# Optimization experiments

Hardware: AMD Instinct MI355X
Metric: run time of the kernel (lower is better)

Reference implementation:

```python
import jax, jax.numpy as jnp
import numpy as np

OUT_FEATURES = 4096
IN_FEATURES = 4096
SCALE_EPS = 1e-5


def setup_inputs() -> dict:
    key = jax.random.key(0)
    k1, k2, k3 = jax.random.split(key, 3)
    x = jax.random.normal(k1, (8192, IN_FEATURES), dtype=jnp.float32)
    # packed int4 weights: two signed nibbles per byte-equivalent int
    weight_packed = jax.random.randint(k2, (OUT_FEATURES, IN_FEATURES // 2), 0, 256, dtype=jnp.int32)
    weight_scale = jax.random.uniform(k3, (OUT_FEATURES,), dtype=jnp.float32) * 0.01 + 1e-4
    return {"x": x, "weight_packed": weight_packed, "weight_scale": weight_scale}


def _unpack_int4(weight_packed):
    # low nibble first, then high nibble, sign-extended from 4 bits
    low = weight_packed & 15
    high = (weight_packed >> 4) & 15
    low = jnp.where(low > 7, low - 16, low)
    high = jnp.where(high > 7, high - 16, high)
    # interleave -> [out_features, in_features]
    w_q = jnp.stack([low, high], axis=-1).reshape(weight_packed.shape[0], -1)
    return w_q


def reference(x, weight_packed, weight_scale):
    # per-row activation quantization to int4 range [-8, 7]
    x_max = jnp.max(jnp.abs(x), axis=-1, keepdims=True)
    x_scale = jnp.maximum(x_max / 7.0, SCALE_EPS)          # [tokens, 1]
    x_q = jnp.clip(jnp.round(x / x_scale), -8.0, 7.0)      # float carrier of int4 values

    w_q = _unpack_int4(weight_packed).astype(jnp.float32)  # [out, in]

    out = jnp.einsum('ti,oi->to', x_q, w_q)                # [tokens, out]
    out = out * (x_scale * weight_scale[None, :])
    return out.astype(x.dtype)
```

## Files before the change

kernel.cpp:

```cpp
#include <hip/hip_runtime.h>

#define SCALE_EPS 1e-5f

typedef int v4i __attribute__((ext_vector_type(4)));

static __device__ __forceinline__ void gll16(const void* g, void* l) {
  __builtin_amdgcn_global_load_lds(
      (const __attribute__((address_space(1))) unsigned int*)g,
      (__attribute__((address_space(3))) unsigned int*)l,
      16, 0, 0);
}

__global__ __launch_bounds__(256) void unpack_w(const int* __restrict__ wp,
                                                char* __restrict__ wq) {
  const int kc = blockIdx.x;
  const int nt = blockIdx.y;
  const int tid = threadIdx.x;
  char* tile = wq + ((size_t)nt * 64 + kc) * 8192;
  const int n0 = nt * 128;
#pragma unroll
  for (int j = 0; j < 4; ++j) {
    int u = j * 256 + tid;
    int r = u >> 3;
    int p = u & 7;
    const v4i* src = (const v4i*)((const char*)wp + (size_t)(n0 + r) * 8192 + kc * 128 + p * 16);
    v4i v = *src;
    unsigned int b[8];
#pragma unroll
    for (int q = 0; q < 4; ++q) {
      int lo = ((v[q] & 15) ^ 8) - 8;
      int hi = (((v[q] >> 4) & 15) ^ 8) - 8;
      b[q * 2]     = (unsigned int)(lo & 255);
      b[q * 2 + 1] = (unsigned int)(hi & 255);
    }
    unsigned int w0 = b[0] | (b[1] << 8) | (b[2] << 16) | (b[3] << 24);
    unsigned int w1 = b[4] | (b[5] << 8) | (b[6] << 16) | (b[7] << 24);
    *(uint2*)(tile + (r >> 4) * 1024 + (p >> 1) * 256 + (r & 15) * 16 + (p & 1) * 8) =
        make_uint2(w0, w1);
  }
}

__global__ __launch_bounds__(256) void quant_x(const float* __restrict__ x,
                                               char* __restrict__ xq,
                                               float* __restrict__ xs) {
  __shared__ float lmax[4][4];
  const int tid = threadIdx.x;
  const int w = tid >> 6;
  const int l = tid & 63;
  const int t0 = blockIdx.x * 4;
  const int row = l >> 4;
  const int t = t0 + row;
  const int sub = l & 15;

  const float* base = x + (size_t)t * 4096 + w * 1024 + sub * 4;
  float4 vals[16];
  float m = 0.0f;
#pragma unroll
  for (int s = 0; s < 16; ++s) {
    vals[s] = *(const float4*)(base + s * 64);
    m = fmaxf(m, fmaxf(fmaxf(fabsf(vals[s].x), fabsf(vals[s].y)),
                       fmaxf(fabsf(vals[s].z), fabsf(vals[s].w))));
  }
#pragma unroll
  for (int d = 1; d < 16; d <<= 1) m = fmaxf(m, __shfl_xor(m, d, 64));
  if (sub == 0) lmax[w][row] = m;
  __syncthreads();
  float rm = fmaxf(fmaxf(lmax[0][row], lmax[1][row]),
                   fmaxf(lmax[2][row], lmax[3][row]));
  float scale = fmaxf(rm / 7.0f, SCALE_EPS);
  if (w == 0 && sub == 0) xs[t] = scale;

  const int mt = t0 >> 7;
  const int f = (t0 & 127) >> 4;
  const int r16 = t & 15;
  const int cc = sub >> 2;
  const int b4 = (sub & 3) * 4;

#pragma unroll
  for (int s = 0; s < 16; ++s) {
    float4 v = vals[s];
    int q0 = (int)fminf(fmaxf(rintf(v.x / scale), -8.0f), 7.0f);
    int q1 = (int)fminf(fmaxf(rintf(v.y / scale), -8.0f), 7.0f);
    int q2 = (int)fminf(fmaxf(rintf(v.z / scale), -8.0f), 7.0f);
    int q3 = (int)fminf(fmaxf(rintf(v.w / scale), -8.0f), 7.0f);
    unsigned int wd = (unsigned int)(q0 & 255) | ((unsigned int)(q1 & 255) << 8) |
                      ((unsigned int)(q2 & 255) << 16) | ((unsigned int)(q3 & 255) << 24);
    *(unsigned int*)(xq + ((size_t)mt * 64 + w * 16 + s) * 8192 +
                     f * 1024 + cc * 256 + r16 * 16 + b4) = wd;
  }
}

__global__ __launch_bounds__(512, 2) void gemm_i8(const char* __restrict__ xq,
                                                  const char* __restrict__ wq,
                                                  const float* __restrict__ xs,
                                                  const float* __restrict__ wsc,
                                                  float* __restrict__ out) {
  __shared__ char lds[4][32768];
  const int tid = threadIdx.x;
  const int wid = tid >> 6;
  const int lane = tid & 63;
  const int wm = wid >> 2;
  const int wn = wid & 3;

  const int bid = blockIdx.x;
  const int wg = (bid & 7) * 64 + (bid >> 3);
  const int by = wg >> 4;
  const int bx = wg & 15;

  const char* Asrc0 = xq + (size_t)(2 * by) * 64 * 8192;
  const char* Asrc1 = Asrc0 + 64 * 8192;
  const char* Bsrc0 = wq + (size_t)(2 * bx) * 64 * 8192;
  const char* Bsrc1 = Bsrc0 + 64 * 8192;
  const int toff = tid * 16;

  v4i acc[8][4] = {};
  v4i fB[2][4];
  v4i aA0, aA1, aA2, aA3;

#define STAGE4(kt)                                                      \
  do {                                                                  \
    char* dst_ = lds[(kt) & 3] + toff;                                  \
    gll16(Asrc0 + (size_t)(kt) * 8192 + toff, dst_);                    \
    gll16(Asrc1 + (size_t)(kt) * 8192 + toff, dst_ + 8192);             \
    gll16(Bsrc0 + (size_t)(kt) * 8192 + toff, dst_ + 16384);            \
    gll16(Bsrc1 + (size_t)(kt) * 8192 + toff, dst_ + 24576);            \
  } while (0)

#define MF2(m0, m1, x, y, c)                                                          \
  do {                                                                                \
    __builtin_amdgcn_s_setprio(1);                                                    \
    _Pragma("unroll") for (int ni = 0; ni < 4; ++ni) {                                \
      acc[m0][ni] =                                                                   \
          __builtin_amdgcn_mfma_i32_16x16x64_i8(x, fB[c][ni], acc[m0][ni], 0, 0, 0);  \
      acc[m1][ni] =                                                                   \
          __builtin_amdgcn_mfma_i32_16x16x64_i8(y, fB[c][ni], acc[m1][ni], 0, 0, 0);  \
    }                                                                                 \
    __builtin_amdgcn_s_setprio(0);                                                    \
  } while (0)

#define TILE(c, kt, do_stage, do_next, vm)                                   \
  do {                                                                       \
    const char* As_ = lds[(kt) & 3] + wm * 8192 + lane * 16;                 \
    const char* Bn_ = lds[((kt) + 1) & 3] + 16384 + wn * 4096 + lane * 16;   \
    const char* An_ = lds[((kt) + 1) & 3] + wm * 8192 + lane * 16;           \
                                 \
    aA2 = *(const v4i*)(As_ + 2048);                                         \
    aA3 = *(const v4i*)(As_ + 3072);                                         \
    MF2(0, 1, aA0, aA1, c);                                                  \
                                 \
    aA0 = *(const v4i*)(As_ + 4096);                                         \
    aA1 = *(const v4i*)(As_ + 5120);                                         \
    MF2(2, 3, aA2, aA3, c);                                                  \
                      \
    if ((vm) == 4) asm volatile("s_waitcnt vmcnt(4)" ::: "memory");          \
    else if ((vm) == 0) asm volatile("s_waitcnt vmcnt(0)" ::: "memory");     \
    __builtin_amdgcn_s_barrier();                                            \
    __builtin_amdgcn_sched_barrier(0);                                       \
       \
    if (do_stage) STAGE4((kt) + 3);                                          \
    aA2 = *(const v4i*)(As_ + 6144);                                         \
    aA3 = *(const v4i*)(As_ + 7168);                                         \
    if (do_next) {                                                           \
      fB[1 - (c)][0] = *(const v4i*)(Bn_);                                   \
      fB[1 - (c)][1] = *(const v4i*)(Bn_ + 1024);                            \
    }                                                                        \
    MF2(4, 5, aA0, aA1, c);                                                  \
             \
    if (do_next) {                                                           \
      fB[1 - (c)][2] = *(const v4i*)(Bn_ + 2048);                            \
      fB[1 - (c)][3] = *(const v4i*)(Bn_ + 3072);                            \
      aA0 = *(const v4i*)(An_);                                              \
      aA1 = *(const v4i*)(An_ + 1024);                                       \
    }                                                                        \
    MF2(6, 7, aA2, aA3, c);                                                  \
  } while (0)

  STAGE4(0); STAGE4(1); STAGE4(2);
  asm volatile("s_waitcnt vmcnt(8)" ::: "memory");
  __builtin_amdgcn_s_barrier();
  __builtin_amdgcn_sched_barrier(0);
  {
    const char* As_ = lds[0] + wm * 8192 + lane * 16;
    const char* Bs_ = lds[0] + 16384 + wn * 4096 + lane * 16;
    aA0 = *(const v4i*)(As_);
    aA1 = *(const v4i*)(As_ + 1024);
    fB[0][0] = *(const v4i*)(Bs_);
    fB[0][1] = *(const v4i*)(Bs_ + 1024);
    fB[0][2] = *(const v4i*)(Bs_ + 2048);
    fB[0][3] = *(const v4i*)(Bs_ + 3072);
  }

  for (int kt = 0; kt < 60; kt += 2) {
    TILE(0, kt, 1, 1, 4);
    TILE(1, kt + 1, 1, 1, 4);
  }
  TILE(0, 60, 1, 1, 4);
  TILE(1, 61, 0, 1, 4);
  TILE(0, 62, 0, 1, 0);
  TILE(1, 63, 0, 0, -1);

#undef TILE
#undef MF2
#undef STAGE4

  float wvv[4];
#pragma unroll
  for (int ni = 0; ni < 4; ++ni)
    wvv[ni] = wsc[bx * 256 + wn * 64 + ni * 16 + (lane & 15)];
  const int rbase = by * 256 + wm * 128 + ((lane >> 4) << 2);
  const int cbase = bx * 256 + wn * 64 + (lane & 15);
#pragma unroll
  for (int mi = 0; mi < 8; ++mi) {
#pragma unroll
    for (int j = 0; j < 4; ++j) {
      int t = rbase + mi * 16 + j;
      float xsv = xs[t];
      float* orow = out + (size_t)t * 4096 + cbase;
#pragma unroll
      for (int ni = 0; ni < 4; ++ni)
        orow[ni * 16] = (float)acc[mi][ni][j] * (xsv * wvv[ni]);
    }
  }
}

extern "C" void kernel_launch(void* const* d_in, const int* in_sizes, int n_in,
                              void* d_out, int out_size, void* d_ws, size_t ws_size,
                              hipStream_t stream) {
  const float* x = (const float*)d_in[0];
  const int* wp = (const int*)d_in[1];
  const float* wsc = (const float*)d_in[2];
  float* out = (float*)d_out;
  char* ws = (char*)d_ws;

  char* xq = ws;
  char* wq = ws + 33554432;
  float* xs = (float*)(ws + 33554432 + 16777216);

  hipLaunchKernelGGL(unpack_w, dim3(64, 32), dim3(256), 0, stream, wp, wq);
  hipLaunchKernelGGL(quant_x, dim3(2048), dim3(256), 0, stream, x, xq, xs);
  hipLaunchKernelGGL(gemm_i8, dim3(512), dim3(512), 0, stream, xq, wq, xs, wsc, out);
}
```

Baseline: 172.8 us.

## Store operands as packed unsigned nibbles and unpack in GEMM with zero-point correction

Activations and weights are now stored in the workspace as offset-binary 4-bit nibbles (value+8), two per byte, which halves global and LDS traffic for the GEMM operands. The GEMM unpacks them with mask and shift into unsigned bytes just before the int8 MFMAs. It then corrects the result using per-row and per-column sums: acc - 8*(sa+sw) + 64*4096. This adds a new sum_w kernel, row-sum reduction in quant_x, and extra ALU work in the GEMM inner loop, in exchange for half the staging bandwidth and smaller LDS buffers.

```diff
diff --git a/kernel.cpp b/kernel.cpp
--- a/kernel.cpp
+++ b/kernel.cpp
@@ -11,39 +11,64 @@
       16, 0, 0);
 }
 
+
 __global__ __launch_bounds__(256) void unpack_w(const int* __restrict__ wp,
                                                 char* __restrict__ wq) {
   const int kc = blockIdx.x;
   const int nt = blockIdx.y;
   const int tid = threadIdx.x;
-  char* tile = wq + ((size_t)nt * 64 + kc) * 8192;
+  char* tile = wq + ((size_t)nt * 64 + kc) * 4096;
   const int n0 = nt * 128;
 #pragma unroll
+  for (int gi = 0; gi < 2; ++gi) {
+    int g = gi * 256 + tid;
+    int r = g >> 2, cc = g & 3;
+    const v4i* src = (const v4i*)(wp + (size_t)(n0 + r) * 2048 + kc * 32 + cc * 8);
+    v4i m0 = src[0], m1 = src[1];
+    unsigned int d0 =
+        ((unsigned)m0.x & 15) | (((unsigned)m0.z & 15) << 4) |
+        ((((unsigned)m0.x >> 4) & 15) << 8) | ((((unsigned)m0.z >> 4) & 15) << 12) |
+        (((unsigned)m0.y & 15) << 16) | (((unsigned)m0.w & 15) << 20) |
+        ((((unsigned)m0.y >> 4) & 15) << 24) | ((((unsigned)m0.w >> 4) & 15) << 28);
+    unsigned int d1 =
+        ((unsigned)m1.x & 15) | (((unsigned)m1.z & 15) << 4) |
+        ((((unsigned)m1.x >> 4) & 15) << 8) | ((((unsigned)m1.z >> 4) & 15) << 12) |
+        (((unsigned)m1.y & 15) << 16) | (((unsigned)m1.w & 15) << 20) |
+        ((((unsigned)m1.y >> 4) & 15) << 24) | ((((unsigned)m1.w >> 4) & 15) << 28);
+    d0 ^= 0x88888888u;
+    d1 ^= 0x88888888u;
+    *(uint2*)(tile + (r >> 5) * 1024 + cc * 256 + (r & 15) * 16 + ((r >> 4) & 1) * 8) =
+        make_uint2(d0, d1);
+  }
+}
+
+__global__ __launch_bounds__(256) void sum_w(const int* __restrict__ wp,
+                                             int* __restrict__ sw) {
+  __shared__ int ls[4];
+  const int row = blockIdx.x;
+  const int tid = threadIdx.x;
+  const v4i* src = (const v4i*)(wp + (size_t)row * 2048 + tid * 8);
+  v4i m0 = src[0], m1 = src[1];
+  int s = 0;
+#pragma unroll
   for (int j = 0; j < 4; ++j) {
-    int u = j * 256 + tid;
-    int r = u >> 3;
-    int p = u & 7;
-    const v4i* src = (const v4i*)((const char*)wp + (size_t)(n0 + r) * 8192 + kc * 128 + p * 16);
-    v4i v = *src;
-    unsigned int b[8];
-#pragma unroll
-    for (int q = 0; q < 4; ++q) {
-      int lo = ((v[q] & 15) ^ 8) - 8;
-      int hi = (((v[q] >> 4) & 15) ^ 8) - 8;
-      b[q * 2]     = (unsigned int)(lo & 255);
-      b[q * 2 + 1] = (unsigned int)(hi & 255);
-    }
-    unsigned int w0 = b[0] | (b[1] << 8) | (b[2] << 16) | (b[3] << 24);
-    unsigned int w1 = b[4] | (b[5] << 8) | (b[6] << 16) | (b[7] << 24);
-    *(uint2*)(tile + (r >> 4) * 1024 + (p >> 1) * 256 + (r & 15) * 16 + (p & 1) * 8) =
-        make_uint2(w0, w1);
-  }
+    int a = (j == 0) ? m0.x : (j == 1) ? m0.y : (j == 2) ? m0.z : m0.w;
+    int b = (j == 0) ? m1.x : (j == 1) ? m1.y : (j == 2) ? m1.z : m1.w;
+    s += ((a & 15) ^ 8) + (((a >> 4) & 15) ^ 8) + ((b & 15) ^ 8) + (((b >> 4) & 15) ^ 8);
+  }
+#pragma unroll
+  for (int d = 1; d < 64; d <<= 1) s += __shfl_xor(s, d, 64);
+  if ((tid & 63) == 0) ls[tid >> 6] = s;
+  __syncthreads();
+  if (tid == 0) sw[row] = ls[0] + ls[1] + ls[2] + ls[3];
 }
 
 __global__ __launch_bounds__(256) void quant_x(const float* __restrict__ x,
                                                char* __restrict__ xq,
-                                               float* __restrict__ xs) {
+                                               float* __restrict__ xs,
+                                               int* __restrict__ sa) {
   __shared__ float lmax[4][4];
+  __shared__ int lsum[4][4];
   const int tid = threadIdx.x;
   const int w = tid >> 6;
   const int l = tid & 63;
@@ -52,14 +77,17 @@
   const int t = t0 + row;
   const int sub = l & 15;
 
-  const float* base = x + (size_t)t * 4096 + w * 1024 + sub * 4;
-  float4 vals[16];
+  const float* base = x + (size_t)t * 4096 + w * 1024 + sub * 8;
+  float4 va[8], vb[8];
   float m = 0.0f;
 #pragma unroll
-  for (int s = 0; s < 16; ++s) {
-    vals[s] = *(const float4*)(base + s * 64);
-    m = fmaxf(m, fmaxf(fmaxf(fabsf(vals[s].x), fabsf(vals[s].y)),
-                       fmaxf(fabsf(vals[s].z), fabsf(vals[s].w))));
+  for (int s = 0; s < 8; ++s) {
+    va[s] = *(const float4*)(base + s * 128);
+    vb[s] = *(const float4*)(base + s * 128 + 4);
+    m = fmaxf(m, fmaxf(fmaxf(fabsf(va[s].x), fabsf(va[s].y)),
+                       fmaxf(fabsf(va[s].z), fabsf(va[s].w))));
+    m = fmaxf(m, fmaxf(fmaxf(fabsf(vb[s].x), fabsf(vb[s].y)),
+                       fmaxf(fabsf(vb[s].z), fabsf(vb[s].w))));
   }
 #pragma unroll
   for (int d = 1; d < 16; d <<= 1) m = fmaxf(m, __shfl_xor(m, d, 64));
@@ -70,32 +98,47 @@
   float scale = fmaxf(rm / 7.0f, SCALE_EPS);
   if (w == 0 && sub == 0) xs[t] = scale;
 
-  const int mt = t0 >> 7;
-  const int f = (t0 & 127) >> 4;
+  const int mt = t >> 7;
+  const int f = (t & 127) >> 4;
   const int r16 = t & 15;
-  const int cc = sub >> 2;
-  const int b4 = (sub & 3) * 4;
-
-#pragma unroll
-  for (int s = 0; s < 16; ++s) {
-    float4 v = vals[s];
-    int q0 = (int)fminf(fmaxf(rintf(v.x / scale), -8.0f), 7.0f);
-    int q1 = (int)fminf(fmaxf(rintf(v.y / scale), -8.0f), 7.0f);
-    int q2 = (int)fminf(fmaxf(rintf(v.z / scale), -8.0f), 7.0f);
-    int q3 = (int)fminf(fmaxf(rintf(v.w / scale), -8.0f), 7.0f);
-    unsigned int wd = (unsigned int)(q0 & 255) | ((unsigned int)(q1 & 255) << 8) |
-                      ((unsigned int)(q2 & 255) << 16) | ((unsigned int)(q3 & 255) << 24);
-    *(unsigned int*)(xq + ((size_t)mt * 64 + w * 16 + s) * 8192 +
-                     f * 1024 + cc * 256 + r16 * 16 + b4) = wd;
-  }
+  const int cc = (sub >> 1) & 3;
+  const int d = sub & 1;
+  char* dst0 = xq + (size_t)(mt * 64) * 4096 +
+               (f >> 1) * 1024 + cc * 256 + r16 * 16 + (f & 1) * 8 + d * 4;
+
+  int isum = 0;
+#pragma unroll
+  for (int s = 0; s < 8; ++s) {
+    int q0 = (int)fminf(fmaxf(rintf(va[s].x / scale), -8.0f), 7.0f) + 8;
+    int q1 = (int)fminf(fmaxf(rintf(va[s].y / scale), -8.0f), 7.0f) + 8;
+    int q2 = (int)fminf(fmaxf(rintf(va[s].z / scale), -8.0f), 7.0f) + 8;
+    int q3 = (int)fminf(fmaxf(rintf(va[s].w / scale), -8.0f), 7.0f) + 8;
+    int q4 = (int)fminf(fmaxf(rintf(vb[s].x / scale), -8.0f), 7.0f) + 8;
+    int q5 = (int)fminf(fmaxf(rintf(vb[s].y / scale), -8.0f), 7.0f) + 8;
+    int q6 = (int)fminf(fmaxf(rintf(vb[s].z / scale), -8.0f), 7.0f) + 8;
+    int q7 = (int)fminf(fmaxf(rintf(vb[s].w / scale), -8.0f), 7.0f) + 8;
+    isum += q0 + q1 + q2 + q3 + q4 + q5 + q6 + q7;
+    unsigned int dw = (unsigned)(q0 | (q4 << 4)) | ((unsigned)(q1 | (q5 << 4)) << 8) |
+                      ((unsigned)(q2 | (q6 << 4)) << 16) | ((unsigned)(q3 | (q7 << 4)) << 24);
+    int kc = w * 16 + s * 2 + (sub >> 3);
+    *(unsigned int*)(dst0 + (size_t)kc * 4096) = dw;
+  }
+#pragma unroll
+  for (int dd = 1; dd < 16; dd <<= 1) isum += __shfl_xor(isum, dd, 64);
+  if (sub == 0) lsum[w][row] = isum;
+  __syncthreads();
+  if (w == 0 && sub == 0)
+    sa[t] = lsum[0][row] + lsum[1][row] + lsum[2][row] + lsum[3][row];
 }
 
 __global__ __launch_bounds__(512, 2) void gemm_i8(const char* __restrict__ xq,
                                                   const char* __restrict__ wq,
                                                   const float* __restrict__ xs,
+                                                  const int* __restrict__ sa,
+                                                  const int* __restrict__ sw,
                                                   const float* __restrict__ wsc,
                                                   float* __restrict__ out) {
-  __shared__ char lds[4][32768];
+  __shared__ char lds[4][16384];
   const int tid = threadIdx.x;
   const int wid = tid >> 6;
   const int lane = tid & 63;
@@ -107,106 +150,119 @@
   const int by = wg >> 4;
   const int bx = wg & 15;
 
-  const char* Asrc0 = xq + (size_t)(2 * by) * 64 * 8192;
-  const char* Asrc1 = Asrc0 + 64 * 8192;
-  const char* Bsrc0 = wq + (size_t)(2 * bx) * 64 * 8192;
-  const char* Bsrc1 = Bsrc0 + 64 * 8192;
   const int toff = tid * 16;
+  const int h = toff >> 12;
+  const int off = toff & 4095;
+  const char* aSrcT = xq + (size_t)(2 * by + h) * 262144 + off;
+  const char* bSrcT = wq + (size_t)(2 * bx + h) * 262144 + off;
+  const int aoff = (lane >> 4) * 256 + (lane & 15) * 16;
 
   v4i acc[8][4] = {};
   v4i fB[2][4];
-  v4i aA0, aA1, aA2, aA3;
-
-#define STAGE4(kt)                                                      \
-  do {                                                                  \
-    char* dst_ = lds[(kt) & 3] + toff;                                  \
-    gll16(Asrc0 + (size_t)(kt) * 8192 + toff, dst_);                    \
-    gll16(Asrc1 + (size_t)(kt) * 8192 + toff, dst_ + 8192);             \
-    gll16(Bsrc0 + (size_t)(kt) * 8192 + toff, dst_ + 16384);            \
-    gll16(Bsrc1 + (size_t)(kt) * 8192 + toff, dst_ + 24576);            \
+  v4i pA0, pA1, pB0, pB1;
+  v4i ua0, ua1, ua2, ua3;
+
+#define LO4(w) (int)((unsigned)(w) & 0x0f0f0f0fu)
+#define HI4(w) (int)(((unsigned)(w) >> 4) & 0x0f0f0f0fu)
+#define UNPK(da, db, p)                                   \
+  do {                                                    \
+    da = (v4i){LO4((p).x), HI4((p).x), LO4((p).y), HI4((p).y)}; \
+    db = (v4i){LO4((p).z), HI4((p).z), LO4((p).w), HI4((p).w)}; \
   } while (0)
 
-#define MF2(m0, m1, x, y, c)                                                          \
-  do {                                                                                \
-    __builtin_amdgcn_s_setprio(1);                                                    \
-    _Pragma("unroll") for (int ni = 0; ni < 4; ++ni) {                                \
-      acc[m0][ni] =                                                                   \
-          __builtin_amdgcn_mfma_i32_16x16x64_i8(x, fB[c][ni], acc[m0][ni], 0, 0, 0);  \
-      acc[m1][ni] =                                                                   \
-          __builtin_amdgcn_mfma_i32_16x16x64_i8(y, fB[c][ni], acc[m1][ni], 0, 0, 0);  \
-    }                                                                                 \
-    __builtin_amdgcn_s_setprio(0);                                                    \
+#define STAGE2(kt)                                        \
+  do {                                                    \
+    char* d_ = lds[(kt) & 3] + toff;                      \
+    gll16(aSrcT + (size_t)(kt) * 4096, d_);               \
+    gll16(bSrcT + (size_t)(kt) * 4096, d_ + 8192);        \
+  } while (0)
+
+#define MF2(m0, m1, xx, yy, c)                                                         \
+  do {                                                                                 \
+    __builtin_amdgcn_s_setprio(1);                                                     \
+    _Pragma("unroll") for (int ni = 0; ni < 4; ++ni) {                                 \
+      acc[m0][ni] =                                                                    \
+          __builtin_amdgcn_mfma_i32_16x16x64_i8(xx, fB[c][ni], acc[m0][ni], 0, 0, 0);  \
+      acc[m1][ni] =                                                                    \
+          __builtin_amdgcn_mfma_i32_16x16x64_i8(yy, fB[c][ni], acc[m1][ni], 0, 0, 0);  \
+    }                                                                                  \
+    __builtin_amdgcn_s_setprio(0);                                                     \
   } while (0)
 
 #define TILE(c, kt, do_stage, do_next, vm)                                   \
   do {                                                                       \
-    const char* As_ = lds[(kt) & 3] + wm * 8192 + lane * 16;                 \
-    const char* Bn_ = lds[((kt) + 1) & 3] + 16384 + wn * 4096 + lane * 16;   \
-    const char* An_ = lds[((kt) + 1) & 3] + wm * 8192 + lane * 16;           \
-                                 \
-    aA2 = *(const v4i*)(As_ + 2048);                                         \
-    aA3 = *(const v4i*)(As_ + 3072);                                         \
-    MF2(0, 1, aA0, aA1, c);                                                  \
-                                 \
-    aA0 = *(const v4i*)(As_ + 4096);                                         \
-    aA1 = *(const v4i*)(As_ + 5120);                                         \
-    MF2(2, 3, aA2, aA3, c);                                                  \
-                      \
-    if ((vm) == 4) asm volatile("s_waitcnt vmcnt(4)" ::: "memory");          \
+    const char* Aw_ = lds[(kt) & 3] + wm * 4096 + aoff;                      \
+    const char* Bn_ = lds[((kt) + 1) & 3] + 8192 + wn * 2048 + aoff;         \
+    const char* An_ = lds[((kt) + 1) & 3] + wm * 4096 + aoff;                \
+                                \
+    pA1 = *(const v4i*)(Aw_ + 1024);                                         \
+    UNPK(ua0, ua1, pA0);                                                     \
+    MF2(0, 1, ua0, ua1, c);                                                  \
+                                \
+    pA0 = *(const v4i*)(Aw_ + 2048);                                         \
+    UNPK(ua2, ua3, pA1);                                                     \
+    MF2(2, 3, ua2, ua3, c);                                                  \
+                           \
+    if ((vm) == 2) asm volatile("s_waitcnt vmcnt(2)" ::: "memory");          \
     else if ((vm) == 0) asm volatile("s_waitcnt vmcnt(0)" ::: "memory");     \
     __builtin_amdgcn_s_barrier();                                            \
     __builtin_amdgcn_sched_barrier(0);                                       \
+          \
+    if (do_stage) STAGE2((kt) + 3);                                          \
+    pA1 = *(const v4i*)(Aw_ + 3072);                                         \
+    if (do_next) pB0 = *(const v4i*)(Bn_);                                   \
+    UNPK(ua0, ua1, pA0);                                                     \
+    MF2(4, 5, ua0, ua1, c);                                                  \
        \
-    if (do_stage) STAGE4((kt) + 3);                                          \
-    aA2 = *(const v4i*)(As_ + 6144);                                         \
-    aA3 = *(const v4i*)(As_ + 7168);                                         \
     if (do_next) {                                                           \
-      fB[1 - (c)][0] = *(const v4i*)(Bn_);                                   \
-      fB[1 - (c)][1] = *(const v4i*)(Bn_ + 1024);                            \
+      pB1 = *(const v4i*)(Bn_ + 1024);                                       \
+      pA0 = *(const v4i*)(An_);                                              \
     }                                                                        \
-    MF2(4, 5, aA0, aA1, c);                                                  \
-             \
+    UNPK(ua2, ua3, pA1);                                                     \
+    MF2(6, 7, ua2, ua3, c);                                                  \
     if (do_next) {                                                           \
-      fB[1 - (c)][2] = *(const v4i*)(Bn_ + 2048);                            \
-      fB[1 - (c)][3] = *(const v4i*)(Bn_ + 3072);                            \
-      aA0 = *(const v4i*)(An_);                                              \
-      aA1 = *(const v4i*)(An_ + 1024);                                       \
+      UNPK(fB[1 - (c)][0], fB[1 - (c)][1], pB0);                             \
+      UNPK(fB[1 - (c)][2], fB[1 - (c)][3], pB1);                             \
     }                                                                        \
-    MF2(6, 7, aA2, aA3, c);                                                  \
   } while (0)
 
-  STAGE4(0); STAGE4(1); STAGE4(2);
-  asm volatile("s_waitcnt vmcnt(8)" ::: "memory");
+  STAGE2(0); STAGE2(1); STAGE2(2);
+  asm volatile("s_waitcnt vmcnt(4)" ::: "memory");
   __builtin_amdgcn_s_barrier();
   __builtin_amdgcn_sched_barrier(0);
   {
-    const char* As_ = lds[0] + wm * 8192 + lane * 16;
-    const char* Bs_ = lds[0] + 16384 + wn * 4096 + lane * 16;
-    aA0 = *(const v4i*)(As_);
-    aA1 = *(const v4i*)(As_ + 1024);
-    fB[0][0] = *(const v4i*)(Bs_);
-    fB[0][1] = *(const v4i*)(Bs_ + 1024);
-    fB[0][2] = *(const v4i*)(Bs_ + 2048);
-    fB[0][3] = *(const v4i*)(Bs_ + 3072);
+    const char* B0_ = lds[0] + 8192 + wn * 2048 + aoff;
+    pB0 = *(const v4i*)(B0_);
+    pB1 = *(const v4i*)(B0_ + 1024);
+    pA0 = *(const v4i*)(lds[0] + wm * 4096 + aoff);
+    UNPK(fB[0][0], fB[0][1], pB0);
+    UNPK(fB[0][2], fB[0][3], pB1);
   }
 
   for (int kt = 0; kt < 60; kt += 2) {
-    TILE(0, kt, 1, 1, 4);
-    TILE(1, kt + 1, 1, 1, 4);
-  }
-  TILE(0, 60, 1, 1, 4);
-  TILE(1, 61, 0, 1, 4);
+    TILE(0, kt, 1, 1, 2);
+    TILE(1, kt + 1, 1, 1, 2);
+  }
+  TILE(0, 60, 1, 1, 2);
+  TILE(1, 61, 0, 1, 2);
   TILE(0, 62, 0, 1, 0);
   TILE(1, 63, 0, 0, -1);
 
 #undef TILE
 #undef MF2
-#undef STAGE4
-
+#undef STAGE2
+#undef UNPK
+#undef LO4
+#undef HI4
+
+  int swv[4];
   float wvv[4];
 #pragma unroll
-  for (int ni = 0; ni < 4; ++ni)
-    wvv[ni] = wsc[bx * 256 + wn * 64 + ni * 16 + (lane & 15)];
+  for (int ni = 0; ni < 4; ++ni) {
+    int col = bx * 256 + wn * 64 + ni * 16 + (lane & 15);
+    swv[ni] = sw[col];
+    wvv[ni] = wsc[col];
+  }
   const int rbase = by * 256 + wm * 128 + ((lane >> 4) << 2);
   const int cbase = bx * 256 + wn * 64 + (lane & 15);
 #pragma unroll
@@ -214,11 +270,14 @@
 #pragma unroll
     for (int j = 0; j < 4; ++j) {
       int t = rbase + mi * 16 + j;
+      int sat = sa[t];
       float xsv = xs[t];
       float* orow = out + (size_t)t * 4096 + cbase;
 #pragma unroll
-      for (int ni = 0; ni < 4; ++ni)
-        orow[ni * 16] = (float)acc[mi][ni][j] * (xsv * wvv[ni]);
+      for (int ni = 0; ni < 4; ++ni) {
+        int cv = acc[mi][ni][j] - 8 * (sat + swv[ni]) + 262144;
+        orow[ni * 16] = (float)cv * (xsv * wvv[ni]);
+      }
     }
   }
 }
@@ -233,10 +292,13 @@
   char* ws = (char*)d_ws;
 
   char* xq = ws;
-  char* wq = ws + 33554432;
-  float* xs = (float*)(ws + 33554432 + 16777216);
+  char* wq = ws + 16777216;
+  float* xs = (float*)(ws + 25165824);
+  int* sa = (int*)(ws + 25165824 + 32768);
+  int* sw = (int*)(ws + 25165824 + 65536);
 
   hipLaunchKernelGGL(unpack_w, dim3(64, 32), dim3(256), 0, stream, wp, wq);
-  hipLaunchKernelGGL(quant_x, dim3(2048), dim3(256), 0, stream, x, xq, xs);
-  hipLaunchKernelGGL(gemm_i8, dim3(512), dim3(512), 0, stream, xq, wq, xs, wsc, out);
-}
+  hipLaunchKernelGGL(sum_w, dim3(4096), dim3(256), 0, stream, wp, sw);
+  hipLaunchKernelGGL(quant_x, dim3(2048), dim3(256), 0, stream, x, xq, xs, sa);
+  hipLaunchKernelGGL(gemm_i8, dim3(512), dim3(512), 0, stream, xq, wq, xs, sa, sw, wsc, out);
+}
```

Result: faster. 165.0 us (-4.5%).

## Keep weights as biased 4-bit nibbles in workspace, unpack in GEMM registers

Applied to the files above, without the earlier changes.

The weight preprocessing now stores weights as unsigned 4-bit nibbles offset by 8, halving the weight workspace and the global-to-LDS traffic per K tile. The GEMM unpacks nibbles to int8 in registers with mask and shift after loading from LDS. It corrects the bias by subtracting 8 times each row's quantized activation sum, which the quantize kernel now computes. This cuts the memory traffic and LDS footprint for B but adds VALU unpack work inside the MFMA loop.

```diff
diff --git a/kernel.cpp b/kernel.cpp
--- a/kernel.cpp
+++ b/kernel.cpp
@@ -11,39 +11,43 @@
       16, 0, 0);
 }
 
+
 __global__ __launch_bounds__(256) void unpack_w(const int* __restrict__ wp,
                                                 char* __restrict__ wq) {
   const int kc = blockIdx.x;
   const int nt = blockIdx.y;
   const int tid = threadIdx.x;
-  char* tile = wq + ((size_t)nt * 64 + kc) * 8192;
+  char* tile = wq + ((size_t)nt * 64 + kc) * 4096;
   const int n0 = nt * 128;
 #pragma unroll
-  for (int j = 0; j < 4; ++j) {
-    int u = j * 256 + tid;
-    int r = u >> 3;
-    int p = u & 7;
-    const v4i* src = (const v4i*)((const char*)wp + (size_t)(n0 + r) * 8192 + kc * 128 + p * 16);
-    v4i v = *src;
-    unsigned int b[8];
-#pragma unroll
-    for (int q = 0; q < 4; ++q) {
-      int lo = ((v[q] & 15) ^ 8) - 8;
-      int hi = (((v[q] >> 4) & 15) ^ 8) - 8;
-      b[q * 2]     = (unsigned int)(lo & 255);
-      b[q * 2 + 1] = (unsigned int)(hi & 255);
-    }
-    unsigned int w0 = b[0] | (b[1] << 8) | (b[2] << 16) | (b[3] << 24);
-    unsigned int w1 = b[4] | (b[5] << 8) | (b[6] << 16) | (b[7] << 24);
-    *(uint2*)(tile + (r >> 4) * 1024 + (p >> 1) * 256 + (r & 15) * 16 + (p & 1) * 8) =
-        make_uint2(w0, w1);
+  for (int gi = 0; gi < 2; ++gi) {
+    int g = gi * 256 + tid;
+    int r = g >> 2, cc = g & 3;
+    const v4i* src = (const v4i*)(wp + (size_t)(n0 + r) * 2048 + kc * 32 + cc * 8);
+    v4i m0 = src[0], m1 = src[1];
+    unsigned int d0 =
+        ((unsigned)m0.x & 15) | (((unsigned)m0.z & 15) << 4) |
+        ((((unsigned)m0.x >> 4) & 15) << 8) | ((((unsigned)m0.z >> 4) & 15) << 12) |
+        (((unsigned)m0.y & 15) << 16) | (((unsigned)m0.w & 15) << 20) |
+        ((((unsigned)m0.y >> 4) & 15) << 24) | ((((unsigned)m0.w >> 4) & 15) << 28);
+    unsigned int d1 =
+        ((unsigned)m1.x & 15) | (((unsigned)m1.z & 15) << 4) |
+        ((((unsigned)m1.x >> 4) & 15) << 8) | ((((unsigned)m1.z >> 4) & 15) << 12) |
+        (((unsigned)m1.y & 15) << 16) | (((unsigned)m1.w & 15) << 20) |
+        ((((unsigned)m1.y >> 4) & 15) << 24) | ((((unsigned)m1.w >> 4) & 15) << 28);
+    d0 ^= 0x88888888u;
+    d1 ^= 0x88888888u;
+    *(uint2*)(tile + (r >> 5) * 1024 + cc * 256 + (r & 15) * 16 + ((r >> 4) & 1) * 8) =
+        make_uint2(d0, d1);
   }
 }
 
 __global__ __launch_bounds__(256) void quant_x(const float* __restrict__ x,
                                                char* __restrict__ xq,
-                                               float* __restrict__ xs) {
+                                               float* __restrict__ xs,
+                                               int* __restrict__ sa) {
   __shared__ float lmax[4][4];
+  __shared__ int lsum[4][4];
   const int tid = threadIdx.x;
   const int w = tid >> 6;
   const int l = tid & 63;
@@ -76,6 +80,7 @@
   const int cc = sub >> 2;
   const int b4 = (sub & 3) * 4;
 
+  int isum = 0;
 #pragma unroll
   for (int s = 0; s < 16; ++s) {
     float4 v = vals[s];
@@ -83,19 +88,27 @@
     int q1 = (int)fminf(fmaxf(rintf(v.y / scale), -8.0f), 7.0f);
     int q2 = (int)fminf(fmaxf(rintf(v.z / scale), -8.0f), 7.0f);
     int q3 = (int)fminf(fmaxf(rintf(v.w / scale), -8.0f), 7.0f);
+    isum += q0 + q1 + q2 + q3;
     unsigned int wd = (unsigned int)(q0 & 255) | ((unsigned int)(q1 & 255) << 8) |
                       ((unsigned int)(q2 & 255) << 16) | ((unsigned int)(q3 & 255) << 24);
     *(unsigned int*)(xq + ((size_t)mt * 64 + w * 16 + s) * 8192 +
                      f * 1024 + cc * 256 + r16 * 16 + b4) = wd;
   }
+#pragma unroll
+  for (int dd = 1; dd < 16; dd <<= 1) isum += __shfl_xor(isum, dd, 64);
+  if (sub == 0) lsum[w][row] = isum;
+  __syncthreads();
+  if (w == 0 && sub == 0)
+    sa[t] = lsum[0][row] + lsum[1][row] + lsum[2][row] + lsum[3][row];
 }
 
 __global__ __launch_bounds__(512, 2) void gemm_i8(const char* __restrict__ xq,
                                                   const char* __restrict__ wq,
                                                   const float* __restrict__ xs,
+                                                  const int* __restrict__ sa,
                                                   const float* __restrict__ wsc,
                                                   float* __restrict__ out) {
-  __shared__ char lds[4][32768];
+  __shared__ char lds[4][24576];
   const int tid = threadIdx.x;
   const int wid = tid >> 6;
   const int lane = tid & 63;
@@ -107,101 +120,113 @@
   const int by = wg >> 4;
   const int bx = wg & 15;
 
-  const char* Asrc0 = xq + (size_t)(2 * by) * 64 * 8192;
-  const char* Asrc1 = Asrc0 + 64 * 8192;
-  const char* Bsrc0 = wq + (size_t)(2 * bx) * 64 * 8192;
-  const char* Bsrc1 = Bsrc0 + 64 * 8192;
   const int toff = tid * 16;
+  const char* aSrc0 = xq + (size_t)(2 * by) * 64 * 8192;
+  const char* aSrc1 = aSrc0 + 64 * 8192;
+  const char* bSrcT = wq + (size_t)(2 * bx + (toff >> 12)) * 262144 + (toff & 4095);
+  const int aoff = (lane >> 4) * 256 + (lane & 15) * 16;
+  const int laoff = lane * 16;
 
   v4i acc[8][4] = {};
   v4i fB[2][4];
   v4i aA0, aA1, aA2, aA3;
-
-#define STAGE4(kt)                                                      \
-  do {                                                                  \
-    char* dst_ = lds[(kt) & 3] + toff;                                  \
-    gll16(Asrc0 + (size_t)(kt) * 8192 + toff, dst_);                    \
-    gll16(Asrc1 + (size_t)(kt) * 8192 + toff, dst_ + 8192);             \
-    gll16(Bsrc0 + (size_t)(kt) * 8192 + toff, dst_ + 16384);            \
-    gll16(Bsrc1 + (size_t)(kt) * 8192 + toff, dst_ + 24576);            \
-  } while (0)
-
-#define MF2(m0, m1, x, y, c)                                                          \
-  do {                                                                                \
-    __builtin_amdgcn_s_setprio(1);                                                    \
-    _Pragma("unroll") for (int ni = 0; ni < 4; ++ni) {                                \
-      acc[m0][ni] =                                                                   \
-          __builtin_amdgcn_mfma_i32_16x16x64_i8(x, fB[c][ni], acc[m0][ni], 0, 0, 0);  \
-      acc[m1][ni] =                                                                   \
-          __builtin_amdgcn_mfma_i32_16x16x64_i8(y, fB[c][ni], acc[m1][ni], 0, 0, 0);  \
-    }                                                                                 \
-    __builtin_amdgcn_s_setprio(0);                                                    \
+  v4i pB0, pB1;
+  const unsigned MSK = 0x0f0f0f0fu;
+
+#define LO4(w) (int)((unsigned)(w) & MSK)
+#define HI4(w) (int)(((unsigned)(w) >> 4) & MSK)
+#define UNPK(da, db, p)                                         \
+  do {                                                          \
+    da = (v4i){LO4((p).x), HI4((p).x), LO4((p).y), HI4((p).y)}; \
+    db = (v4i){LO4((p).z), HI4((p).z), LO4((p).w), HI4((p).w)}; \
+  } while (0)
+
+#define STAGE3(kt)                                              \
+  do {                                                          \
+    char* d_ = lds[(kt) & 3];                                   \
+    gll16(aSrc0 + (size_t)(kt) * 8192 + toff, d_ + toff);       \
+    gll16(aSrc1 + (size_t)(kt) * 8192 + toff, d_ + 8192 + toff);\
+    gll16(bSrcT + (size_t)(kt) * 4096, d_ + 16384 + toff);      \
+  } while (0)
+
+#define MF2(m0, m1, xx, yy, c)                                                         \
+  do {                                                                                 \
+    __builtin_amdgcn_s_setprio(1);                                                     \
+    _Pragma("unroll") for (int ni = 0; ni < 4; ++ni) {                                 \
+      acc[m0][ni] =                                                                    \
+          __builtin_amdgcn_mfma_i32_16x16x64_i8(xx, fB[c][ni], acc[m0][ni], 0, 0, 0);  \
+      acc[m1][ni] =                                                                    \
+          __builtin_amdgcn_mfma_i32_16x16x64_i8(yy, fB[c][ni], acc[m1][ni], 0, 0, 0);  \
+    }                                                                                  \
+    __builtin_amdgcn_s_setprio(0);                                                     \
   } while (0)
 
 #define TILE(c, kt, do_stage, do_next, vm)                                   \
   do {                                                                       \
-    const char* As_ = lds[(kt) & 3] + wm * 8192 + lane * 16;                 \
-    const char* Bn_ = lds[((kt) + 1) & 3] + 16384 + wn * 4096 + lane * 16;   \
-    const char* An_ = lds[((kt) + 1) & 3] + wm * 8192 + lane * 16;           \
-                                 \
-    aA2 = *(const v4i*)(As_ + 2048);                                         \
-    aA3 = *(const v4i*)(As_ + 3072);                                         \
+    const char* Aw_ = lds[(kt) & 3] + wm * 8192 + laoff;                     \
+    const char* Bn_ = lds[((kt) + 1) & 3] + 16384 + wn * 2048 + aoff;        \
+    const char* An_ = lds[((kt) + 1) & 3] + wm * 8192 + laoff;               \
+                                  \
+    aA2 = *(const v4i*)(Aw_ + 2048);                                         \
+    aA3 = *(const v4i*)(Aw_ + 3072);                                         \
     MF2(0, 1, aA0, aA1, c);                                                  \
-                                 \
-    aA0 = *(const v4i*)(As_ + 4096);                                         \
-    aA1 = *(const v4i*)(As_ + 5120);                                         \
+                                  \
+    aA0 = *(const v4i*)(Aw_ + 4096);                                         \
+    aA1 = *(const v4i*)(Aw_ + 5120);                                         \
     MF2(2, 3, aA2, aA3, c);                                                  \
-                      \
-    if ((vm) == 4) asm volatile("s_waitcnt vmcnt(4)" ::: "memory");          \
+                            \
+    if ((vm) == 3) asm volatile("s_waitcnt vmcnt(3)" ::: "memory");          \
     else if ((vm) == 0) asm volatile("s_waitcnt vmcnt(0)" ::: "memory");     \
     __builtin_amdgcn_s_barrier();                                            \
     __builtin_amdgcn_sched_barrier(0);                                       \
-       \
-    if (do_stage) STAGE4((kt) + 3);                                          \
-    aA2 = *(const v4i*)(As_ + 6144);                                         \
-    aA3 = *(const v4i*)(As_ + 7168);                                         \
+        \
+    if (do_stage) STAGE3((kt) + 3);                                          \
+    aA2 = *(const v4i*)(Aw_ + 6144);                                         \
+    aA3 = *(const v4i*)(Aw_ + 7168);                                         \
+    if (do_next) pB0 = *(const v4i*)(Bn_);                                   \
+    MF2(4, 5, aA0, aA1, c);                                                  \
+     \
     if (do_next) {                                                           \
-      fB[1 - (c)][0] = *(const v4i*)(Bn_);                                   \
-      fB[1 - (c)][1] = *(const v4i*)(Bn_ + 1024);                            \
-    }                                                                        \
-    MF2(4, 5, aA0, aA1, c);                                                  \
-             \
-    if (do_next) {                                                           \
-      fB[1 - (c)][2] = *(const v4i*)(Bn_ + 2048);                            \
-      fB[1 - (c)][3] = *(const v4i*)(Bn_ + 3072);                            \
+      pB1 = *(const v4i*)(Bn_ + 1024);                                       \
       aA0 = *(const v4i*)(An_);                                              \
       aA1 = *(const v4i*)(An_ + 1024);                                       \
     }                                                                        \
     MF2(6, 7, aA2, aA3, c);                                                  \
-  } while (0)
-
-  STAGE4(0); STAGE4(1); STAGE4(2);
-  asm volatile("s_waitcnt vmcnt(8)" ::: "memory");
+    if (do_next) {                                                           \
+      UNPK(fB[1 - (c)][0], fB[1 - (c)][1], pB0);                             \
+      UNPK(fB[1 - (c)][2], fB[1 - (c)][3], pB1);                             \
+    }                                                                        \
+  } while (0)
+
+  STAGE3(0); STAGE3(1); STAGE3(2);
+  asm volatile("s_waitcnt vmcnt(6)" ::: "memory");
   __builtin_amdgcn_s_barrier();
   __builtin_amdgcn_sched_barrier(0);
   {
-    const char* As_ = lds[0] + wm * 8192 + lane * 16;
-    const char* Bs_ = lds[0] + 16384 + wn * 4096 + lane * 16;
-    aA0 = *(const v4i*)(As_);
-    aA1 = *(const v4i*)(As_ + 1024);
-    fB[0][0] = *(const v4i*)(Bs_);
-    fB[0][1] = *(const v4i*)(Bs_ + 1024);
-    fB[0][2] = *(const v4i*)(Bs_ + 2048);
-    fB[0][3] = *(const v4i*)(Bs_ + 3072);
+    const char* B0_ = lds[0] + 16384 + wn * 2048 + aoff;
+    pB0 = *(const v4i*)(B0_);
+    pB1 = *(const v4i*)(B0_ + 1024);
+    aA0 = *(const v4i*)(lds[0] + wm * 8192 + laoff);
+    aA1 = *(const v4i*)(lds[0] + wm * 8192 + laoff + 1024);
+    UNPK(fB[0][0], fB[0][1], pB0);
+    UNPK(fB[0][2], fB[0][3], pB1);
   }
 
   for (int kt = 0; kt < 60; kt += 2) {
-    TILE(0, kt, 1, 1, 4);
-    TILE(1, kt + 1, 1, 1, 4);
-  }
-  TILE(0, 60, 1, 1, 4);
-  TILE(1, 61, 0, 1, 4);
+    TILE(0, kt, 1, 1, 3);
+    TILE(1, kt + 1, 1, 1, 3);
+  }
+  TILE(0, 60, 1, 1, 3);
+  TILE(1, 61, 0, 1, 3);
   TILE(0, 62, 0, 1, 0);
   TILE(1, 63, 0, 0, -1);
 
 #undef TILE
 #undef MF2
-#undef STAGE4
+#undef STAGE3
+#undef UNPK
+#undef LO4
+#undef HI4
 
   float wvv[4];
 #pragma unroll
@@ -214,11 +239,14 @@
 #pragma unroll
     for (int j = 0; j < 4; ++j) {
       int t = rbase + mi * 16 + j;
+      int sat = sa[t];
       float xsv = xs[t];
       float* orow = out + (size_t)t * 4096 + cbase;
 #pragma unroll
-      for (int ni = 0; ni < 4; ++ni)
-        orow[ni * 16] = (float)acc[mi][ni][j] * (xsv * wvv[ni]);
+      for (int ni = 0; ni < 4; ++ni) {
+        int cv = acc[mi][ni][j] - 8 * sat;
+        orow[ni * 16] = (float)cv * (xsv * wvv[ni]);
+      }
     }
   }
 }
@@ -234,9 +262,10 @@
 
   char* xq = ws;
   char* wq = ws + 33554432;
-  float* xs = (float*)(ws + 33554432 + 16777216);
+  float* xs = (float*)(ws + 41943040);
+  int* sa = (int*)(ws + 41943040 + 32768);
 
   hipLaunchKernelGGL(unpack_w, dim3(64, 32), dim3(256), 0, stream, wp, wq);
-  hipLaunchKernelGGL(quant_x, dim3(2048), dim3(256), 0, stream, x, xq, xs);
-  hipLaunchKernelGGL(gemm_i8, dim3(512), dim3(512), 0, stream, xq, wq, xs, wsc, out);
-}
+  hipLaunchKernelGGL(quant_x, dim3(2048), dim3(256), 0, stream, x, xq, xs, sa);
+  hipLaunchKernelGGL(gemm_i8, dim3(512), dim3(512), 0, stream, xq, wq, xs, sa, wsc, out);
+}
```

Result: faster. 168.2 us (-2.7%).
